# Optimization experiments

Measured on AMD Instinct MI355X. Metric: run time of the kernel, lower is better.

## Reference

```python
import jax, jax.numpy as jnp
import numpy as np

LOWERSIZE = 40


def setup_inputs() -> dict:
    key = jax.random.key(0)
    ks = jax.random.split(key, 6)
    N, x_dim, y_dim = 2048, 768, 768
    return {
        "x_samples": jax.random.normal(ks[0], (N, x_dim), dtype=jnp.float32),
        "y_samples": jax.random.normal(ks[1], (N, y_dim), dtype=jnp.float32),
        "W1": jax.random.normal(ks[2], (LOWERSIZE, x_dim + y_dim), dtype=jnp.float32) * 0.02,
        "b1": jax.random.normal(ks[3], (LOWERSIZE,), dtype=jnp.float32) * 0.02,
        "W2": jax.random.normal(ks[4], (1, LOWERSIZE), dtype=jnp.float32) * 0.02,
        "b2": jax.random.normal(ks[5], (1,), dtype=jnp.float32) * 0.02,
    }


def reference(x_samples, y_samples, W1, b1, W2, b2):
    # F(z) = W2 @ relu(W1 @ z + b1) + b2, z = cat(x, y)
    N = y_samples.shape[0]
    x_dim = x_samples.shape[1]
    W1x = W1[:, :x_dim]   # [40, x_dim]
    W1y = W1[:, x_dim:]   # [40, y_dim]

    # Diagonal term T0: F(cat(x_i, y_i)) -> [N, 1]
    h0 = jax.nn.relu(x_samples @ W1x.T + y_samples @ W1y.T + b1)
    T0 = h0 @ W2.T + b2

    # Pairwise term: T1[i, j] = F(cat(x_j, y_i)) - 1.
    # Split the first Linear over x and y to avoid materializing the
    # [N, N, x_dim+y_dim] concatenation (same math, linearity of W1).
    hx = x_samples @ W1x.T  # [N, 40]
    hy = y_samples @ W1y.T  # [N, 40]
    h = jax.nn.relu(hy[:, None, :] + hx[None, :, :] + b1)  # [N, N, 40]
    T1 = (h @ W2.T + b2 - 1.0)[..., 0]  # [N, N]

    lse = jax.nn.logsumexp(T1, axis=1) - jnp.log(jnp.float32(N))  # [N]
    lower_bound = T0.mean() - jnp.exp(lse).mean()
    return lower_bound
```

## Files before the change

### kernel.cpp

```cpp
#include <hip/hip_runtime.h>

#define NROWS 2048
#define KDIM  768
#define L     40
#define KCH   6
#define KCSZ  128
#define HN    (NROWS * L)

#define PSTR 328

__global__ __launch_bounds__(256) void k_proj(const float* __restrict__ x,
                                              const float* __restrict__ y,
                                              const float* __restrict__ W1,
                                              float* __restrict__ part) {
    const int kc    = blockIdx.y;
    const int which = blockIdx.z;
    const float* __restrict__ A = which ? y : x;
    const int tid = threadIdx.x;
    const int r   = tid >> 4;
    const int seg = tid & 15;
    const int row0 = blockIdx.x * 32;

    __shared__ float sh[32 * PSTR];

    const float* arowA = A + (size_t)(row0 + r) * KDIM + kc * KCSZ;
    const float* arowB = A + (size_t)(row0 + 16 + r) * KDIM + kc * KCSZ;
    float4 a0 = *(const float4*)(arowA + seg * 4);
    float4 a1 = *(const float4*)(arowA + 64 + seg * 4);
    float4 b0 = *(const float4*)(arowB + seg * 4);
    float4 b1 = *(const float4*)(arowB + 64 + seg * 4);

    const float* wbase = W1 + (size_t)which * KDIM + kc * KCSZ;
#pragma unroll 8
    for (int o = 0; o < L; ++o) {
        const float* wrow = wbase + (size_t)o * (2 * KDIM);
        float4 w0 = *(const float4*)(wrow + seg * 4);
        float4 w1 = *(const float4*)(wrow + 64 + seg * 4);
        float sA = a0.x * w0.x + a0.y * w0.y + a0.z * w0.z + a0.w * w0.w
                 + a1.x * w1.x + a1.y * w1.y + a1.z * w1.z + a1.w * w1.w;
        float sB = b0.x * w0.x + b0.y * w0.y + b0.z * w0.z + b0.w * w0.w
                 + b1.x * w1.x + b1.y * w1.y + b1.z * w1.z + b1.w * w1.w;
        sA += __shfl_xor(sA, 8);
        sB += __shfl_xor(sB, 8);
        if (seg < 8) {
            sh[r * PSTR + o * 8 + seg] = sA;
            sh[(r + 16) * PSTR + o * 8 + seg] = sB;
        }
    }
    __syncthreads();

    float* pout = part + (size_t)(kc * 2 + which) * HN + (size_t)row0 * L;
#pragma unroll
    for (int k = 0; k < 5; ++k) {
        int idx = tid + k * 256;
        int rr = idx / L;
        int o  = idx - rr * L;
        const float4* p = (const float4*)(sh + rr * PSTR + o * 8);
        float4 u0 = p[0], u1 = p[1];
        pout[idx] = u0.x + u0.y + u0.z + u0.w + u1.x + u1.y + u1.z + u1.w;
    }
}

__global__ __launch_bounds__(256) void k_red(const float* __restrict__ part,
                                             const float* __restrict__ b1,
                                             float* __restrict__ hxb,
                                             float* __restrict__ hy) {
    int gid = blockIdx.x * 256 + threadIdx.x;
    int which = gid / HN;
    int rem   = gid - which * HN;
    float s = 0.f;
#pragma unroll
    for (int kc = 0; kc < KCH; ++kc)
        s += part[(size_t)(kc * 2 + which) * HN + rem];
    if (!which) {
        s += b1[rem % L];
        hxb[rem] = s;
    } else {
        hy[rem] = s;
    }
}

#define BI 128
#define BJ 64
#define STRD 44

__global__ __launch_bounds__(512, 4) void k_pair(const float* __restrict__ hxb,
                                                 const float* __restrict__ hy,
                                                 const float* __restrict__ W2,
                                                 const float* __restrict__ b2p,
                                                 float* __restrict__ pairE,
                                                 float* __restrict__ pairT) {
    __shared__ float shy[BI * STRD];
    __shared__ float shx[BJ * STRD];
    __shared__ float sw2[STRD];
    __shared__ float red[16];

    const int tid = threadIdx.x;
    const int i0 = blockIdx.x * BI;
    const int j0 = blockIdx.y * BJ;

    for (int idx = tid; idx < BI * 10; idx += 512) {
        int rr = idx / 10, c = idx - rr * 10;
        float4 v = ((const float4*)(hy + (size_t)i0 * L))[idx];
        *(float4*)(shy + rr * STRD + c * 4) = v;
    }
    for (int idx = tid; idx < BJ * 10; idx += 512) {
        int rr = idx / 10, c = idx - rr * 10;
        float4 v = ((const float4*)(hxb + (size_t)j0 * L))[idx];
        *(float4*)(shx + rr * STRD + c * 4) = v;
    }
    if (tid < 10) ((float4*)sw2)[tid] = ((const float4*)W2)[tid];
    __syncthreads();

    const int tx = tid & 15, ty = tid >> 4;

    float acc[4][4];
#pragma unroll
    for (int u = 0; u < 4; ++u)
#pragma unroll
        for (int v = 0; v < 4; ++v) acc[u][v] = 0.f;

    float4 ayA[4], axA[4], wA4;
    float4 ayB[4], axB[4], wB4;

#define LOADF(AY, AX, W4, K4) do {                                          \
    W4 = *(const float4*)(sw2 + (K4) * 4);                                  \
    _Pragma("unroll") for (int u_ = 0; u_ < 4; ++u_)                        \
        AY[u_] = *(const float4*)(shy + (ty + 32 * u_) * STRD + (K4) * 4);  \
    _Pragma("unroll") for (int v_ = 0; v_ < 4; ++v_)                        \
        AX[v_] = *(const float4*)(shx + (tx + 16 * v_) * STRD + (K4) * 4);  \
} while (0)

#define FMAF(AY, AX, W4) do {                                               \
    _Pragma("unroll") for (int u_ = 0; u_ < 4; ++u_)                        \
    _Pragma("unroll") for (int v_ = 0; v_ < 4; ++v_) {                      \
        float t;                                                            \
        t = AY[u_].x + AX[v_].x; t = fmaxf(t, 0.f); acc[u_][v_] += t * W4.x;\
        t = AY[u_].y + AX[v_].y; t = fmaxf(t, 0.f); acc[u_][v_] += t * W4.y;\
        t = AY[u_].z + AX[v_].z; t = fmaxf(t, 0.f); acc[u_][v_] += t * W4.z;\
        t = AY[u_].w + AX[v_].w; t = fmaxf(t, 0.f); acc[u_][v_] += t * W4.w;\
    }                                                                       \
} while (0)

    LOADF(ayA, axA, wA4, 0);
    LOADF(ayB, axB, wB4, 1);
    FMAF(ayA, axA, wA4); LOADF(ayA, axA, wA4, 2);
    FMAF(ayB, axB, wB4); LOADF(ayB, axB, wB4, 3);
    FMAF(ayA, axA, wA4); LOADF(ayA, axA, wA4, 4);
    FMAF(ayB, axB, wB4); LOADF(ayB, axB, wB4, 5);
    FMAF(ayA, axA, wA4); LOADF(ayA, axA, wA4, 6);
    FMAF(ayB, axB, wB4); LOADF(ayB, axB, wB4, 7);
    FMAF(ayA, axA, wA4); LOADF(ayA, axA, wA4, 8);
    FMAF(ayB, axB, wB4); LOADF(ayB, axB, wB4, 9);
    FMAF(ayA, axA, wA4);
    FMAF(ayB, axB, wB4);

#undef LOADF
#undef FMAF

    const float b2v = b2p[0];
    const float c1  = b2v - 1.f;
    float sumE = 0.f, sumT = 0.f;
#pragma unroll
    for (int u = 0; u < 4; ++u)
#pragma unroll
        for (int v = 0; v < 4; ++v) {
            int gi = i0 + ty + 32 * u;
            int gj = j0 + tx + 16 * v;
            float val = acc[u][v];
            if (gi == gj) sumT += val + b2v;
            sumE += __expf(val + c1);
        }

#pragma unroll
    for (int off = 32; off > 0; off >>= 1) {
        sumE += __shfl_down(sumE, off);
        sumT += __shfl_down(sumT, off);
    }
    int wid = tid >> 6;
    if ((tid & 63) == 0) { red[wid] = sumE; red[8 + wid] = sumT; }
    __syncthreads();
    if (tid == 0) {
        float e = 0.f, t = 0.f;
#pragma unroll
        for (int q = 0; q < 8; ++q) { e += red[q]; t += red[8 + q]; }
        int bid = blockIdx.y * gridDim.x + blockIdx.x;
        pairE[bid] = e;
        pairT[bid] = t;
    }
}

__global__ __launch_bounds__(512) void k_fin(const float* __restrict__ pairE,
                                             const float* __restrict__ pairT,
                                             float* __restrict__ out) {
    __shared__ float red[16];
    const int tid = threadIdx.x;
    float e = pairE[tid];
    float t = pairT[tid];
#pragma unroll
    for (int off = 32; off > 0; off >>= 1) {
        e += __shfl_down(e, off);
        t += __shfl_down(t, off);
    }
    int wid = tid >> 6;
    if ((tid & 63) == 0) { red[wid] = e; red[8 + wid] = t; }
    __syncthreads();
    if (tid == 0) {
        float se = 0.f, st = 0.f;
#pragma unroll
        for (int q = 0; q < 8; ++q) { se += red[q]; st += red[8 + q]; }
        const float invN = 1.0f / (float)NROWS;
        out[0] = st * invN - se * invN * invN;
    }
}

extern "C" void kernel_launch(void* const* d_in, const int* in_sizes, int n_in,
                              void* d_out, int out_size, void* d_ws, size_t ws_size,
                              hipStream_t stream) {
    const float* x  = (const float*)d_in[0];
    const float* y  = (const float*)d_in[1];
    const float* W1 = (const float*)d_in[2];
    const float* b1 = (const float*)d_in[3];
    const float* W2 = (const float*)d_in[4];
    const float* b2 = (const float*)d_in[5];
    float* out = (float*)d_out;

    float* wsf   = (float*)d_ws;
    float* hxb   = wsf;
    float* hy    = hxb + HN;
    float* part  = hy + HN;
    float* pairE = part + (size_t)KCH * 2 * HN;
    float* pairT = pairE + 512;

    k_proj<<<dim3(NROWS / 32, KCH, 2), 256, 0, stream>>>(x, y, W1, part);
    k_red<<<(2 * HN) / 256, 256, 0, stream>>>(part, b1, hxb, hy);
    k_pair<<<dim3(NROWS / BI, NROWS / BJ), 512, 0, stream>>>(hxb, hy, W2, b2, pairE, pairT);
    k_fin<<<1, 512, 0, stream>>>(pairE, pairT, out);
}
```

Measured before the change: 101.0 us.

## Fuse split-K projection and reduction into one projection kernel

The projection kernel now has each thread hold a full 768-wide row slice in registers and accumulate all six K chunks itself, so the partial-sum buffer and the separate reduction kernel go away. The cross-thread reduction is done in shared memory with a padded stride, and the bias is added in the same pass. This removes one kernel launch and the round trip of twelve partial buffers through global memory. The cost is higher register pressure (12 float4 per thread) and fewer blocks (256 instead of 768), which lowers parallelism.

```diff
diff --git a/kernel.cpp b/kernel.cpp
--- a/kernel.cpp
+++ b/kernel.cpp
@@ -3,80 +3,58 @@
 #define NROWS 2048
 #define KDIM  768
 #define L     40
-#define KCH   6
-#define KCSZ  128
 #define HN    (NROWS * L)
-
-#define PSTR 328
 
 __global__ __launch_bounds__(256) void k_proj(const float* __restrict__ x,
                                               const float* __restrict__ y,
                                               const float* __restrict__ W1,
-                                              float* __restrict__ part) {
-    const int kc    = blockIdx.y;
-    const int which = blockIdx.z;
+                                              const float* __restrict__ b1,
+                                              float* __restrict__ hxb,
+                                              float* __restrict__ hy) {
+    const int which = blockIdx.y;
     const float* __restrict__ A = which ? y : x;
     const int tid = threadIdx.x;
     const int r   = tid >> 4;
     const int seg = tid & 15;
-    const int row0 = blockIdx.x * 32;
-
-    __shared__ float sh[32 * PSTR];
-
-    const float* arowA = A + (size_t)(row0 + r) * KDIM + kc * KCSZ;
-    const float* arowB = A + (size_t)(row0 + 16 + r) * KDIM + kc * KCSZ;
-    float4 a0 = *(const float4*)(arowA + seg * 4);
-    float4 a1 = *(const float4*)(arowA + 64 + seg * 4);
-    float4 b0 = *(const float4*)(arowB + seg * 4);
-    float4 b1 = *(const float4*)(arowB + 64 + seg * 4);
-
-    const float* wbase = W1 + (size_t)which * KDIM + kc * KCSZ;
-#pragma unroll 8
+    const int row0 = blockIdx.x * 16;
+
+    __shared__ float sh[16 * 688];
+
+    const float* arow = A + (size_t)(row0 + r) * KDIM;
+    float4 a[12];
+#pragma unroll
+    for (int kc = 0; kc < 6; ++kc) {
+        a[2 * kc]     = *(const float4*)(arow + kc * 128 + seg * 4);
+        a[2 * kc + 1] = *(const float4*)(arow + kc * 128 + 64 + seg * 4);
+    }
+
+    const float* wbase = W1 + (size_t)which * KDIM;
+#pragma unroll 4
     for (int o = 0; o < L; ++o) {
         const float* wrow = wbase + (size_t)o * (2 * KDIM);
-        float4 w0 = *(const float4*)(wrow + seg * 4);
-        float4 w1 = *(const float4*)(wrow + 64 + seg * 4);
-        float sA = a0.x * w0.x + a0.y * w0.y + a0.z * w0.z + a0.w * w0.w
-                 + a1.x * w1.x + a1.y * w1.y + a1.z * w1.z + a1.w * w1.w;
-        float sB = b0.x * w0.x + b0.y * w0.y + b0.z * w0.z + b0.w * w0.w
-                 + b1.x * w1.x + b1.y * w1.y + b1.z * w1.z + b1.w * w1.w;
-        sA += __shfl_xor(sA, 8);
-        sB += __shfl_xor(sB, 8);
-        if (seg < 8) {
-            sh[r * PSTR + o * 8 + seg] = sA;
-            sh[(r + 16) * PSTR + o * 8 + seg] = sB;
+        float s = 0.f;
+#pragma unroll
+        for (int kc = 0; kc < 6; ++kc) {
+            float4 w0 = *(const float4*)(wrow + kc * 128 + seg * 4);
+            float4 w1 = *(const float4*)(wrow + kc * 128 + 64 + seg * 4);
+            float4 a0 = a[2 * kc], a1 = a[2 * kc + 1];
+            s += a0.x * w0.x + a0.y * w0.y + a0.z * w0.z + a0.w * w0.w
+               + a1.x * w1.x + a1.y * w1.y + a1.z * w1.z + a1.w * w1.w;
         }
-    }
-    __syncthreads();
-
-    float* pout = part + (size_t)(kc * 2 + which) * HN + (size_t)row0 * L;
-#pragma unroll
-    for (int k = 0; k < 5; ++k) {
-        int idx = tid + k * 256;
+        sh[r * 688 + o * 17 + seg] = s;
+    }
+    __syncthreads();
+
+    float* pout = (which ? hy : hxb) + (size_t)row0 * L;
+    for (int idx = tid; idx < 16 * L; idx += 256) {
         int rr = idx / L;
         int o  = idx - rr * L;
-        const float4* p = (const float4*)(sh + rr * PSTR + o * 8);
-        float4 u0 = p[0], u1 = p[1];
-        pout[idx] = u0.x + u0.y + u0.z + u0.w + u1.x + u1.y + u1.z + u1.w;
-    }
-}
-
-__global__ __launch_bounds__(256) void k_red(const float* __restrict__ part,
-                                             const float* __restrict__ b1,
-                                             float* __restrict__ hxb,
-                                             float* __restrict__ hy) {
-    int gid = blockIdx.x * 256 + threadIdx.x;
-    int which = gid / HN;
-    int rem   = gid - which * HN;
-    float s = 0.f;
-#pragma unroll
-    for (int kc = 0; kc < KCH; ++kc)
-        s += part[(size_t)(kc * 2 + which) * HN + rem];
-    if (!which) {
-        s += b1[rem % L];
-        hxb[rem] = s;
-    } else {
-        hy[rem] = s;
+        float s = 0.f;
+        int base = rr * 688 + o * 17;
+#pragma unroll
+        for (int q = 0; q < 16; ++q) s += sh[base + q];
+        if (!which) s += b1[o];
+        pout[idx] = s;
     }
 }
 
@@ -228,12 +206,10 @@
     float* wsf   = (float*)d_ws;
     float* hxb   = wsf;
     float* hy    = hxb + HN;
-    float* part  = hy + HN;
-    float* pairE = part + (size_t)KCH * 2 * HN;
+    float* pairE = hy + HN;
     float* pairT = pairE + 512;
 
-    k_proj<<<dim3(NROWS / 32, KCH, 2), 256, 0, stream>>>(x, y, W1, part);
-    k_red<<<(2 * HN) / 256, 256, 0, stream>>>(part, b1, hxb, hy);
+    k_proj<<<dim3(NROWS / 16, 2), 256, 0, stream>>>(x, y, W1, b1, hxb, hy);
     k_pair<<<dim3(NROWS / BI, NROWS / BJ), 512, 0, stream>>>(hxb, hy, W2, b2, pairE, pairT);
     k_fin<<<1, 512, 0, stream>>>(pairE, pairT, out);
 }
```

After: 154.3 us. 1.53x slower.
